# Kernel optimization log

Hardware: AMD Instinct MI355X
Metric: run time of the kernel (lower is better)

The kernel has to match this reference:

```python
import jax, jax.numpy as jnp
from jax import lax
import numpy as np

T, B, I, H = 512, 64, 512, 512


def setup_inputs() -> dict:
    key = jax.random.key(0)
    k0, k1, k2, k3, k4 = jax.random.split(key, 5)
    s = 1.0 / np.sqrt(H)  # PyTorch LSTM init range
    x = jax.random.normal(k0, (T, B, I), dtype=jnp.float32)
    W_ih = jax.random.uniform(k1, (4 * H, I), jnp.float32, -s, s)
    W_hh = jax.random.uniform(k2, (4 * H, H), jnp.float32, -s, s)
    b_ih = jax.random.uniform(k3, (4 * H,), jnp.float32, -s, s)
    b_hh = jax.random.uniform(k4, (4 * H,), jnp.float32, -s, s)
    return {"x": x, "W_ih": W_ih, "W_hh": W_hh, "b_ih": b_ih, "b_hh": b_hh}


def reference(x, W_ih, W_hh, b_ih, b_hh):
    # x: [T, B, I] (seq-first, like nn.LSTM with batch_first=False)
    Bv = x.shape[1]
    Hv = W_hh.shape[1]
    # Precompute input projections for all timesteps: [T, B, 4H]
    x_proj = jnp.einsum('tbi,gi->tbg', x, W_ih) + b_ih + b_hh

    def step(carry, xp):
        h, c = carry
        gates = xp + h @ W_hh.T  # [B, 4H]
        i, f, g, o = jnp.split(gates, 4, axis=-1)  # PyTorch gate order i,f,g,o
        i = jax.nn.sigmoid(i)
        f = jax.nn.sigmoid(f)
        g = jnp.tanh(g)
        o = jax.nn.sigmoid(o)
        c = f * c + i * g
        h = o * jnp.tanh(c)
        return (h, c), h

    h0 = jnp.zeros((Bv, Hv), dtype=x.dtype)
    c0 = jnp.zeros((Bv, Hv), dtype=x.dtype)
    _, ys = lax.scan(step, (h0, c0), x_proj)
    return ys  # [T, B, H]
```

## Files before the change

kernel.cpp:

```cpp
#include <hip/hip_runtime.h>


#define T_STEPS 512
#define BATCH   64
#define HID     512
#define NB      64
#define CNT_STRIDE 16

typedef short bf16x8 __attribute__((ext_vector_type(8)));
typedef float f32x4  __attribute__((ext_vector_type(4)));

struct U16B { unsigned long long x, y; };

__device__ __forceinline__ unsigned short f2bf(float f) {
    unsigned int u = __builtin_bit_cast(unsigned int, f);
    u += 0x7FFFu + ((u >> 16) & 1u);
    return (unsigned short)(u >> 16);
}
__device__ __forceinline__ unsigned int pack2(float lo, float hi) {
    return (unsigned int)f2bf(lo) | ((unsigned int)f2bf(hi) << 16);
}
__device__ __forceinline__ uint4 cvt8(const float* __restrict__ p) {
    float4 f0 = *(const float4*)p;
    float4 f1 = *(const float4*)(p + 4);
    uint4 r;
    r.x = pack2(f0.x, f0.y);
    r.y = pack2(f0.z, f0.w);
    r.z = pack2(f1.x, f1.y);
    r.w = pack2(f1.z, f1.w);
    return r;
}
__device__ __forceinline__ void store_cg16(void* p, uint4 v) {
    unsigned long long* q = (unsigned long long*)p;
    U16B u = __builtin_bit_cast(U16B, v);
    __hip_atomic_store(q,     u.x, __ATOMIC_RELAXED, __HIP_MEMORY_SCOPE_AGENT);
    __hip_atomic_store(q + 1, u.y, __ATOMIC_RELAXED, __HIP_MEMORY_SCOPE_AGENT);
}
__device__ __forceinline__ float sigmoidf_(float x) {
    return 1.0f / (1.0f + __expf(-x));
}
__device__ __forceinline__ float tanhf_(float x) {
    x = fminf(fmaxf(x, -15.f), 15.f);
    float e = __expf(2.0f * x);
    return (e - 1.0f) / (e + 1.0f);
}

extern "C" __global__ void __launch_bounds__(256, 1)
lstm_fused(const float* __restrict__ x,
           const float* __restrict__ W_ih,
           const float* __restrict__ W_hh,
           const float* __restrict__ b_ih,
           const float* __restrict__ b_hh,
           float* __restrict__ out,
           unsigned int* __restrict__ cnt,
           unsigned short* __restrict__ hbuf)
{
    __shared__ uint4 sB[2][2][16][64];
    __shared__ __align__(16) unsigned short sH[4][16][8];
    __shared__ __align__(16) float          sHf[4][16][8];

    const int blk  = blockIdx.x;
    const int tid  = threadIdx.x;
    const int w    = tid >> 6;
    const int lane = tid & 63;
    const int l15  = lane & 15;
    const int quad = lane >> 4;
    const int hc0  = blk * 8;

    for (int u = tid; u < 2 * 16 * 64; u += 256) {
        int nt   = u >> 10;
        int kk   = (u >> 6) & 15;
        int ln   = u & 63;
        int c    = (ln & 15) + (nt << 4);
        int grow = ((c >> 3) << 9) + hc0 + (c & 7);
        int k0   = kk * 32 + ((ln >> 4) << 3);
        sB[0][nt][kk][ln] = cvt8(W_ih + grow * 512 + k0);
        sB[1][nt][kk][ln] = cvt8(W_hh + grow * 512 + k0);
    }

    float bias0, bias1;
    {
        int c0 = l15,      g0 = ((c0 >> 3) << 9) + hc0 + (c0 & 7);
        int c1 = l15 + 16, g1 = ((c1 >> 3) << 9) + hc0 + (c1 & 7);
        bias0 = b_ih[g0] + b_hh[g0];
        bias1 = b_ih[g1] + b_hh[g1];
    }
    __syncthreads();

    float cst[4] = {0.f, 0.f, 0.f, 0.f};
    const int aoff = (((w << 4) + l15) * 512) + (quad << 3);
    char* const hb_base = (char*)hbuf;
    const int   hread_off = (quad << 10) + (((w << 4) + l15) << 4);
    long long budget = 300000LL;

    for (int t = 0; t < T_STEPS; ++t) {
        f32x4 acc0 = {0.f, 0.f, 0.f, 0.f};
        f32x4 acc1 = {0.f, 0.f, 0.f, 0.f};

        const float* xt = x + (size_t)t * (BATCH * 512) + aoff;
#pragma unroll
        for (int kk = 0; kk < 16; ++kk) {
            bf16x8 a  = __builtin_bit_cast(bf16x8, cvt8(xt + kk * 32));
            bf16x8 b0 = __builtin_bit_cast(bf16x8, sB[0][0][kk][lane]);
            bf16x8 b1 = __builtin_bit_cast(bf16x8, sB[0][1][kk][lane]);
            acc0 = __builtin_amdgcn_mfma_f32_16x16x32_bf16(a, b0, acc0, 0, 0, 0);
            acc1 = __builtin_amdgcn_mfma_f32_16x16x32_bf16(a, b1, acc1, 0, 0, 0);
        }

        if (t > 0) {
            if (tid == 0) {
                const unsigned int* cp = cnt + (size_t)(t - 1) * CNT_STRIDE;
                while (budget > 0) {
                    unsigned int v = __hip_atomic_load(cp, __ATOMIC_RELAXED,
                                                       __HIP_MEMORY_SCOPE_AGENT);
                    if (v >= NB) break;
                    __builtin_amdgcn_s_sleep(1);
                    --budget;
                }
            }
            __syncthreads();

            const char* hp = hb_base + (((t - 1) & 1) << 16) + hread_off;
            U16B ha[16];
#pragma unroll
            for (int kk = 0; kk < 16; ++kk) {
                const unsigned long long* q =
                    (const unsigned long long*)(hp + (kk << 12));
                ha[kk].x = __hip_atomic_load(q,     __ATOMIC_RELAXED,
                                             __HIP_MEMORY_SCOPE_AGENT);
                ha[kk].y = __hip_atomic_load(q + 1, __ATOMIC_RELAXED,
                                             __HIP_MEMORY_SCOPE_AGENT);
            }
#pragma unroll
            for (int kk = 0; kk < 16; ++kk) {
                bf16x8 a  = __builtin_bit_cast(bf16x8, ha[kk]);
                bf16x8 b0 = __builtin_bit_cast(bf16x8, sB[1][0][kk][lane]);
                bf16x8 b1 = __builtin_bit_cast(bf16x8, sB[1][1][kk][lane]);
                acc0 = __builtin_amdgcn_mfma_f32_16x16x32_bf16(a, b0, acc0, 0, 0, 0);
                acc1 = __builtin_amdgcn_mfma_f32_16x16x32_bf16(a, b1, acc1, 0, 0, 0);
            }
        }

        float gi[4], gf[4], gg[4], go[4];
#pragma unroll
        for (int r = 0; r < 4; ++r) {
            float a0 = acc0[r] + bias0;
            float a1 = acc1[r] + bias1;
            float p0 = __shfl_xor(a0, 8, 64);
            float p1 = __shfl_xor(a1, 8, 64);
            gi[r] = a0; gg[r] = a1; gf[r] = p0; go[r] = p1;
        }
        if (l15 < 8) {
#pragma unroll
            for (int r = 0; r < 4; ++r) {
                float iv = sigmoidf_(gi[r]);
                float fv = sigmoidf_(gf[r]);
                float gv = tanhf_(gg[r]);
                float ov = sigmoidf_(go[r]);
                cst[r] = fv * cst[r] + iv * gv;
                float hv = ov * tanhf_(cst[r]);
                sH [w][(quad << 2) + r][l15] = f2bf(hv);
                sHf[w][(quad << 2) + r][l15] = hv;
            }
        }
        asm volatile("s_waitcnt lgkmcnt(0)" ::: "memory");
        if (lane < 16) {
            uint4 v = *(const uint4*)&sH[w][lane][0];
            char* dst = hb_base + ((t & 1) << 16) + (blk << 10)
                        + (((w << 4) + lane) << 4);
            store_cg16(dst, v);
        }
        asm volatile("s_waitcnt vmcnt(0)" ::: "memory");
        __syncthreads();
        if (tid == 0) {
            (void)__hip_atomic_fetch_add(cnt + (size_t)t * CNT_STRIDE, 1u,
                                         __ATOMIC_RELAXED, __HIP_MEMORY_SCOPE_AGENT);
        }

        if (lane < 32) {
            int row  = lane & 15;
            int half = lane >> 4;
            uint4 v = *(const uint4*)&sHf[w][row][half << 2];
            float* op = out + (size_t)t * (BATCH * HID)
                        + (size_t)((w << 4) + row) * HID + hc0 + (half << 2);
            *(uint4*)op = v;
        }
    }
}

extern "C" void kernel_launch(void* const* d_in, const int* in_sizes, int n_in,
                              void* d_out, int out_size, void* d_ws, size_t ws_size,
                              hipStream_t stream) {
    const float* x    = (const float*)d_in[0];
    const float* W_ih = (const float*)d_in[1];
    const float* W_hh = (const float*)d_in[2];
    const float* b_ih = (const float*)d_in[3];
    const float* b_hh = (const float*)d_in[4];
    float* out = (float*)d_out;

    unsigned int*   cnt = (unsigned int*)d_ws;
    const size_t    cnt_bytes = (size_t)T_STEPS * CNT_STRIDE * sizeof(unsigned int);
    unsigned short* hbuf = (unsigned short*)((char*)d_ws + cnt_bytes);

    (void)hipMemsetAsync(cnt, 0, cnt_bytes, stream);

    hipLaunchKernelGGL(lstm_fused, dim3(NB), dim3(256), 0, stream,
                       x, W_ih, W_hh, b_ih, b_hh, out, cnt, hbuf);
}
```

Measured before the change: 3.985 ms.

## Hoist input projection into a separate fully parallel pre-kernel

Adds an xproj_kernel that computes x·W_ih^T plus biases for all timesteps across 512 blocks and writes the result to workspace in the MFMA accumulator layout. The recurrent kernel then loads the precomputed gates per step instead of running 16 MFMAs and converting x on its serial critical path. This trades a large workspace buffer (about 256MB), extra write and read traffic, and a second launch for a shorter per-step latency in the 64-block recurrence. It falls back to the old path when the workspace is too small.

```diff
diff --git a/kernel.cpp b/kernel.cpp
--- a/kernel.cpp
+++ b/kernel.cpp
@@ -46,6 +46,66 @@
 }
 
 extern "C" __global__ void __launch_bounds__(256, 1)
+xproj_kernel(const float* __restrict__ x,
+             const float* __restrict__ W_ih,
+             const float* __restrict__ b_ih,
+             const float* __restrict__ b_hh,
+             float* __restrict__ xp)
+{
+    __shared__ uint4 sBi[2][16][64];
+
+    const int bid    = blockIdx.x;
+    const int colblk = bid & 63;
+    const int t0     = (bid >> 6) << 6;
+    const int tid    = threadIdx.x;
+    const int w      = tid >> 6;
+    const int lane   = tid & 63;
+    const int l15    = lane & 15;
+    const int quad   = lane >> 4;
+    const int hc0    = colblk * 8;
+
+    for (int u = tid; u < 2 * 16 * 64; u += 256) {
+        int nt   = u >> 10;
+        int kk   = (u >> 6) & 15;
+        int ln   = u & 63;
+        int c    = (ln & 15) + (nt << 4);
+        int grow = ((c >> 3) << 9) + hc0 + (c & 7);
+        int k0   = kk * 32 + ((ln >> 4) << 3);
+        sBi[nt][kk][ln] = cvt8(W_ih + grow * 512 + k0);
+    }
+    float bias0, bias1;
+    {
+        int c0 = l15,      g0 = ((c0 >> 3) << 9) + hc0 + (c0 & 7);
+        int c1 = l15 + 16, g1 = ((c1 >> 3) << 9) + hc0 + (c1 & 7);
+        bias0 = b_ih[g0] + b_hh[g0];
+        bias1 = b_ih[g1] + b_hh[g1];
+    }
+    __syncthreads();
+
+    const int aoff = (((w << 4) + l15) * 512) + (quad << 3);
+
+    for (int t = t0; t < t0 + 64; ++t) {
+        f32x4 acc0 = {0.f, 0.f, 0.f, 0.f};
+        f32x4 acc1 = {0.f, 0.f, 0.f, 0.f};
+        const float* xt = x + (size_t)t * (BATCH * 512) + aoff;
+#pragma unroll
+        for (int kk = 0; kk < 16; ++kk) {
+            bf16x8 a  = __builtin_bit_cast(bf16x8, cvt8(xt + kk * 32));
+            bf16x8 b0 = __builtin_bit_cast(bf16x8, sBi[0][kk][lane]);
+            bf16x8 b1 = __builtin_bit_cast(bf16x8, sBi[1][kk][lane]);
+            acc0 = __builtin_amdgcn_mfma_f32_16x16x32_bf16(a, b0, acc0, 0, 0, 0);
+            acc1 = __builtin_amdgcn_mfma_f32_16x16x32_bf16(a, b1, acc1, 0, 0, 0);
+        }
+#pragma unroll
+        for (int r = 0; r < 4; ++r) { acc0[r] += bias0; acc1[r] += bias1; }
+
+        float* dst = xp + ((size_t)t * NB + colblk) * 2048 + (w << 8) + (lane << 2);
+        *(float4*)dst          = __builtin_bit_cast(float4, acc0);
+        *(float4*)(dst + 1024) = __builtin_bit_cast(float4, acc1);
+    }
+}
+
+extern "C" __global__ void __launch_bounds__(256, 1)
 lstm_fused(const float* __restrict__ x,
            const float* __restrict__ W_ih,
            const float* __restrict__ W_hh,
@@ -53,7 +113,9 @@
            const float* __restrict__ b_hh,
            float* __restrict__ out,
            unsigned int* __restrict__ cnt,
-           unsigned short* __restrict__ hbuf)
+           unsigned short* __restrict__ hbuf,
+           const float* __restrict__ xp,
+           int use_xp)
 {
     __shared__ uint4 sB[2][2][16][64];
     __shared__ __align__(16) unsigned short sH[4][16][8];
@@ -74,12 +136,12 @@
         int c    = (ln & 15) + (nt << 4);
         int grow = ((c >> 3) << 9) + hc0 + (c & 7);
         int k0   = kk * 32 + ((ln >> 4) << 3);
-        sB[0][nt][kk][ln] = cvt8(W_ih + grow * 512 + k0);
         sB[1][nt][kk][ln] = cvt8(W_hh + grow * 512 + k0);
-    }
-
-    float bias0, bias1;
-    {
+        if (!use_xp) sB[0][nt][kk][ln] = cvt8(W_ih + grow * 512 + k0);
+    }
+
+    float bias0 = 0.f, bias1 = 0.f;
+    if (!use_xp) {
         int c0 = l15,      g0 = ((c0 >> 3) << 9) + hc0 + (c0 & 7);
         int c1 = l15 + 16, g1 = ((c1 >> 3) << 9) + hc0 + (c1 & 7);
         bias0 = b_ih[g0] + b_hh[g0];
@@ -97,14 +159,23 @@
         f32x4 acc0 = {0.f, 0.f, 0.f, 0.f};
         f32x4 acc1 = {0.f, 0.f, 0.f, 0.f};
 
-        const float* xt = x + (size_t)t * (BATCH * 512) + aoff;
-#pragma unroll
-        for (int kk = 0; kk < 16; ++kk) {
-            bf16x8 a  = __builtin_bit_cast(bf16x8, cvt8(xt + kk * 32));
-            bf16x8 b0 = __builtin_bit_cast(bf16x8, sB[0][0][kk][lane]);
-            bf16x8 b1 = __builtin_bit_cast(bf16x8, sB[0][1][kk][lane]);
-            acc0 = __builtin_amdgcn_mfma_f32_16x16x32_bf16(a, b0, acc0, 0, 0, 0);
-            acc1 = __builtin_amdgcn_mfma_f32_16x16x32_bf16(a, b1, acc1, 0, 0, 0);
+        if (use_xp) {
+            const float* xb = xp + ((size_t)t * NB + blk) * 2048
+                              + (w << 8) + (lane << 2);
+            float4 xv0 = *(const float4*)xb;
+            float4 xv1 = *(const float4*)(xb + 1024);
+            acc0 = __builtin_bit_cast(f32x4, xv0);
+            acc1 = __builtin_bit_cast(f32x4, xv1);
+        } else {
+            const float* xt = x + (size_t)t * (BATCH * 512) + aoff;
+#pragma unroll
+            for (int kk = 0; kk < 16; ++kk) {
+                bf16x8 a  = __builtin_bit_cast(bf16x8, cvt8(xt + kk * 32));
+                bf16x8 b0 = __builtin_bit_cast(bf16x8, sB[0][0][kk][lane]);
+                bf16x8 b1 = __builtin_bit_cast(bf16x8, sB[0][1][kk][lane]);
+                acc0 = __builtin_amdgcn_mfma_f32_16x16x32_bf16(a, b0, acc0, 0, 0, 0);
+                acc1 = __builtin_amdgcn_mfma_f32_16x16x32_bf16(a, b1, acc1, 0, 0, 0);
+            }
         }
 
         if (t > 0) {
@@ -198,12 +269,22 @@
     const float* b_hh = (const float*)d_in[4];
     float* out = (float*)d_out;
 
-    unsigned int*   cnt = (unsigned int*)d_ws;
-    const size_t    cnt_bytes = (size_t)T_STEPS * CNT_STRIDE * sizeof(unsigned int);
+    const size_t cnt_bytes  = (size_t)T_STEPS * CNT_STRIDE * sizeof(unsigned int);
+    const size_t hbuf_bytes = (size_t)2 * NB * 64 * 8 * sizeof(unsigned short);
+    const size_t xp_bytes   = (size_t)T_STEPS * NB * 2048 * sizeof(float);
+
+    unsigned int*   cnt  = (unsigned int*)d_ws;
     unsigned short* hbuf = (unsigned short*)((char*)d_ws + cnt_bytes);
+    float*          xp   = (float*)((char*)d_ws + cnt_bytes + hbuf_bytes);
+
+    const int use_xp = (ws_size >= cnt_bytes + hbuf_bytes + xp_bytes) ? 1 : 0;
 
     (void)hipMemsetAsync(cnt, 0, cnt_bytes, stream);
 
+    if (use_xp) {
+        hipLaunchKernelGGL(xproj_kernel, dim3(512), dim3(256), 0, stream,
+                           x, W_ih, b_ih, b_hh, xp);
+    }
     hipLaunchKernelGGL(lstm_fused, dim3(NB), dim3(256), 0, stream,
-                       x, W_ih, W_hh, b_ih, b_hh, out, cnt, hbuf);
-}
+                       x, W_ih, W_hh, b_ih, b_hh, out, cnt, hbuf, xp, use_xp);
+}
```

New measurement: 4.007 ms. No clear change (+0.5%).
